# Optimization experiments

Hardware: AMD Instinct MI355X
Metric: run time of the kernel (lower is better)

Reference implementation:

```python
import jax, jax.numpy as jnp
import numpy as np

EPS = 1e-5


def setup_inputs() -> dict:
    key = jax.random.key(0)
    ks = jax.random.split(key, 6)
    BS, N, C, D, E = 4, 2048, 8, 128, 256
    x = jax.random.normal(ks[0], (BS, N, C, D), dtype=jnp.float32)
    h_prev = jax.random.normal(ks[1], (BS, C, E), dtype=jnp.float32)
    gamma = jnp.ones((C, D), dtype=jnp.float32)
    beta = jnp.zeros((C, D), dtype=jnp.float32)
    w_in = jax.random.normal(ks[2], (C, D, 2 * E), dtype=jnp.float32) * (D ** -0.5)
    b_in = jnp.zeros((C, 2 * E), dtype=jnp.float32)
    w_out = jax.random.normal(ks[3], (C, E, D), dtype=jnp.float32) * (E ** -0.5)
    b_out = jnp.zeros((C, D), dtype=jnp.float32)
    return {"x": x, "h_prev": h_prev, "gamma": gamma, "beta": beta,
            "w_in": w_in, "b_in": b_in, "w_out": w_out, "b_out": b_out}


def _scan_combine(c1, c2):
    # (a1, b1) then (a2, b2): h = a2*(a1*h + b1) + b2
    a1, b1 = c1
    a2, b2 = c2
    return a2 * a1, a2 * b1 + b2


def reference(x, h_prev, gamma, beta, w_in, b_in, w_out, b_out):
    # Grouped LayerNorm over D_col per group c
    mu = jnp.mean(x, axis=-1, keepdims=True)
    var = jnp.mean(jnp.square(x - mu), axis=-1, keepdims=True)
    x_norm = (x - mu) * jax.lax.rsqrt(var + EPS) * gamma + beta  # [BS,N,C,D]

    # Grouped linear in: [BS,N,C,D] x [C,D,2E] -> [BS,N,C,2E]
    ab = jnp.einsum('bncd,cde->bnce', x_norm, w_in) + b_in
    a_raw, b_raw = jnp.split(ab, 2, axis=-1)
    a = jax.nn.sigmoid(a_raw)           # decay gates in [0,1]
    b = jax.nn.silu(b_raw)              # gated inputs

    # Fold initial state into first step: h_1 = a_1*h0 + b_1
    b = b.at[:, 0].add(a[:, 0] * h_prev)

    # Parallel linear recurrence h_t = a_t*h_{t-1} + b_t over time axis
    _, h = jax.lax.associative_scan(_scan_combine, (a, b), axis=1)  # [BS,N,C,E]

    # Grouped linear out + residual
    out = jnp.einsum('bnce,ced->bncd', h, w_out) + b_out + x
    return out, h[:, -1]
```

## Files before the change

### kernel.cpp

```cpp
#include <hip/hip_runtime.h>
#include <hip/hip_bf16.h>

#define BS 4
#define NSEQ 2048
#define C_ 8
#define D_ 128
#define E_ 256
#define TWO_E 512
#define CHUNK 64
#define NCH (NSEQ / CHUNK)

typedef __attribute__((ext_vector_type(8))) short short8;
typedef __attribute__((ext_vector_type(4))) float floatx4;

__device__ __forceinline__ unsigned short f2bf(float f) {
    unsigned int u = __float_as_uint(f);
    return (unsigned short)((u + 0x7FFFu + ((u >> 16) & 1u)) >> 16);
}

__device__ __forceinline__ float sigmoidf_(float v) {
    return 1.0f / (1.0f + __expf(-v));
}

__global__ __launch_bounds__(256) void k_transpose_win(const float* __restrict__ w,
                                                       unsigned short* __restrict__ wt) {
    __shared__ float tile[32][33];
    const int c = blockIdx.z;
    const int d0 = blockIdx.y * 32;
    const int e0 = blockIdx.x * 32;
    const int tx = threadIdx.x, ty = threadIdx.y;
    #pragma unroll
    for (int k = 0; k < 4; k++)
        tile[ty + k * 8][tx] = w[((size_t)(c * D_ + d0 + ty + k * 8)) * TWO_E + e0 + tx];
    __syncthreads();
    #pragma unroll
    for (int k = 0; k < 4; k++)
        wt[((size_t)(c * TWO_E + e0 + ty + k * 8)) * D_ + d0 + tx] = f2bf(tile[tx][ty + k * 8]);
}

__global__ __launch_bounds__(256) void k_transpose_wout(const float* __restrict__ w,
                                                        unsigned short* __restrict__ wt) {
    __shared__ float tile[32][33];
    const int c = blockIdx.z;
    const int e0 = blockIdx.y * 32;
    const int d0 = blockIdx.x * 32;
    const int tx = threadIdx.x, ty = threadIdx.y;
    #pragma unroll
    for (int k = 0; k < 4; k++)
        tile[ty + k * 8][tx] = w[((size_t)(c * E_ + e0 + ty + k * 8)) * D_ + d0 + tx];
    __syncthreads();
    #pragma unroll
    for (int k = 0; k < 4; k++)
        wt[((size_t)(c * D_ + d0 + ty + k * 8)) * E_ + e0 + tx] = f2bf(tile[tx][ty + k * 8]);
}

__global__ __launch_bounds__(256) void k1_ln_gemm_in(
    const float* __restrict__ x, const float* __restrict__ gamma, const float* __restrict__ beta,
    const unsigned short* __restrict__ wt_in, const float* __restrict__ b_in,
    float* __restrict__ ab_buf, float* __restrict__ aggA, float* __restrict__ aggB)
{
    constexpr int LDA = 136;
    __shared__ unsigned short xn[CHUNK * LDA];

    const int gid = blockIdx.x;
    const int j = gid & (NCH - 1);
    const int c = (gid >> 5) & (C_ - 1);
    const int b = gid >> 8;
    const int n0 = j * CHUNK;
    const int tid = threadIdx.x;

    {
        const int r = tid >> 2;
        const int p = tid & 3;
        const float* xrow = x + ((size_t)((b * NSEQ + n0 + r) * C_) + c) * D_;
        float4 xv[8];
        float s = 0.f, ss = 0.f;
        #pragma unroll
        for (int i = 0; i < 8; i++) {
            xv[i] = ((const float4*)xrow)[p + 4 * i];
            s += xv[i].x + xv[i].y + xv[i].z + xv[i].w;
            ss += xv[i].x * xv[i].x + xv[i].y * xv[i].y + xv[i].z * xv[i].z + xv[i].w * xv[i].w;
        }
        s += __shfl_xor(s, 1);  s += __shfl_xor(s, 2);
        ss += __shfl_xor(ss, 1); ss += __shfl_xor(ss, 2);
        const float mu = s * (1.0f / D_);
        const float rsig = rsqrtf(fmaxf(ss * (1.0f / D_) - mu * mu, 0.f) + 1e-5f);
        #pragma unroll
        for (int i = 0; i < 8; i++) {
            const int f = p + 4 * i;
            const float4 g  = ((const float4*)(gamma + c * D_))[f];
            const float4 bt = ((const float4*)(beta + c * D_))[f];
            ushort4 o;
            o.x = f2bf((xv[i].x - mu) * rsig * g.x + bt.x);
            o.y = f2bf((xv[i].y - mu) * rsig * g.y + bt.y);
            o.z = f2bf((xv[i].z - mu) * rsig * g.z + bt.z);
            o.w = f2bf((xv[i].w - mu) * rsig * g.w + bt.w);
            *(ushort4*)&xn[r * LDA + 4 * f] = o;
        }
    }
    __syncthreads();

    const int wave = tid >> 6;
    const int lane = tid & 63;
    const int lrow = lane & 15;
    const int quad = lane >> 4;

    short8 afr[4][4];
    #pragma unroll
    for (int m = 0; m < 4; m++) {
        #pragma unroll
        for (int k = 0; k < 4; k++)
            afr[m][k] = *(const short8*)&xn[(m * 16 + lrow) * LDA + k * 32 + quad * 8];
    }

    const unsigned short* wbase = wt_in + (size_t)c * TWO_E * D_;
    float* abrow0 = ab_buf + ((size_t)(b * C_ + c) * NSEQ + n0) * TWO_E;

    #pragma unroll
    for (int nt = 0; nt < 8; nt++) {
        const int e2 = wave * 128 + nt * 16 + lrow;
        short8 bfr[4];
        #pragma unroll
        for (int k = 0; k < 4; k++)
            bfr[k] = *(const short8*)&wbase[(size_t)e2 * D_ + k * 32 + quad * 8];
        floatx4 acc[4];
        #pragma unroll
        for (int m = 0; m < 4; m++) acc[m] = (floatx4){0.f, 0.f, 0.f, 0.f};
        #pragma unroll
        for (int m = 0; m < 4; m++) {
            #pragma unroll
            for (int k = 0; k < 4; k++)
                acc[m] = __builtin_amdgcn_mfma_f32_16x16x32_bf16(afr[m][k], bfr[k], acc[m], 0, 0, 0);
        }
        const float bias = b_in[c * TWO_E + e2];
        const int col = (e2 < E_) ? (2 * e2) : (2 * (e2 - E_) + 1);
        #pragma unroll
        for (int m = 0; m < 4; m++) {
            #pragma unroll
            for (int rr = 0; rr < 4; rr++) {
                const int row = m * 16 + quad * 4 + rr;
                const float v = acc[m][rr] + bias;
                const float sg = sigmoidf_(v);
                abrow0[(size_t)row * TWO_E + col] = (e2 < E_) ? sg : (v * sg);
            }
        }
    }

    __threadfence_block();
    __syncthreads();

    {
        const int e = tid;
        float A = 1.f, Bv = 0.f;
        const float* pr = abrow0 + 2 * e;
        #pragma unroll 8
        for (int i = 0; i < CHUNK; i++) {
            const float2 v = *(const float2*)&pr[(size_t)i * TWO_E];
            A = v.x * A;
            Bv = v.x * Bv + v.y;
        }
        const size_t o = ((size_t)(b * C_ + c) * NCH + j) * E_ + e;
        aggA[o] = A;
        aggB[o] = Bv;
    }
}

__global__ __launch_bounds__(256) void k2_scan_chunks(
    const float* __restrict__ h_prev, const float* __restrict__ aggA, const float* __restrict__ aggB,
    float* __restrict__ hin, float* __restrict__ h_last)
{
    const int bc = blockIdx.x;
    const int e = threadIdx.x;
    float h = h_prev[(size_t)bc * E_ + e];
    const size_t base = (size_t)bc * NCH * E_ + e;
    #pragma unroll
    for (int jj = 0; jj < NCH; jj++) {
        hin[base + (size_t)jj * E_] = h;
        h = aggA[base + (size_t)jj * E_] * h + aggB[base + (size_t)jj * E_];
    }
    h_last[(size_t)bc * E_ + e] = h;
}

__global__ __launch_bounds__(256) void k3_scan_gemm_out(
    const float* __restrict__ ab_buf, const float* __restrict__ hin,
    const unsigned short* __restrict__ wt_out, const float* __restrict__ b_out,
    const float* __restrict__ x, float* __restrict__ out)
{
    constexpr int LDH = 264;
    __shared__ unsigned short hs[CHUNK * LDH];

    const int gid = blockIdx.x;
    const int j = gid & (NCH - 1);
    const int c = (gid >> 5) & (C_ - 1);
    const int b = gid >> 8;
    const int n0 = j * CHUNK;
    const int tid = threadIdx.x;

    {
        const int e = tid;
        float h = hin[((size_t)(b * C_ + c) * NCH + j) * E_ + e];
        const float* pr = ab_buf + ((size_t)(b * C_ + c) * NSEQ + n0) * TWO_E + 2 * e;
        #pragma unroll
        for (int i = 0; i < CHUNK; i++) {
            const float2 v = *(const float2*)&pr[(size_t)i * TWO_E];
            h = v.x * h + v.y;
            hs[i * LDH + e] = f2bf(h);
        }
    }
    __syncthreads();

    const int wave = tid >> 6;
    const int lane = tid & 63;
    const int lrow = lane & 15;
    const int quad = lane >> 4;
    const int m0 = wave * 16;

    short8 afr[8];
    #pragma unroll
    for (int k = 0; k < 8; k++)
        afr[k] = *(const short8*)&hs[(m0 + lrow) * LDH + k * 32 + quad * 8];

    const unsigned short* wbase = wt_out + (size_t)c * D_ * E_;

    #pragma unroll
    for (int nt = 0; nt < 8; nt++) {
        const int d = nt * 16 + lrow;
        short8 bfr[8];
        #pragma unroll
        for (int k = 0; k < 8; k++)
            bfr[k] = *(const short8*)&wbase[(size_t)d * E_ + k * 32 + quad * 8];
        floatx4 acc = (floatx4){0.f, 0.f, 0.f, 0.f};
        #pragma unroll
        for (int k = 0; k < 8; k++)
            acc = __builtin_amdgcn_mfma_f32_16x16x32_bf16(afr[k], bfr[k], acc, 0, 0, 0);
        const float bias = b_out[c * D_ + d];
        #pragma unroll
        for (int rr = 0; rr < 4; rr++) {
            const int row = m0 + quad * 4 + rr;
            const size_t xi = ((size_t)((b * NSEQ + n0 + row) * C_) + c) * D_ + d;
            out[xi] = acc[rr] + bias + x[xi];
        }
    }
}

extern "C" void kernel_launch(void* const* d_in, const int* in_sizes, int n_in,
                              void* d_out, int out_size, void* d_ws, size_t ws_size,
                              hipStream_t stream) {
    (void)in_sizes; (void)n_in; (void)out_size; (void)ws_size;
    const float* x      = (const float*)d_in[0];
    const float* h_prev = (const float*)d_in[1];
    const float* gamma  = (const float*)d_in[2];
    const float* beta   = (const float*)d_in[3];
    const float* w_in   = (const float*)d_in[4];
    const float* b_in   = (const float*)d_in[5];
    const float* w_out  = (const float*)d_in[6];
    const float* b_out  = (const float*)d_in[7];

    float* out    = (float*)d_out;
    float* h_last = out + (size_t)BS * NSEQ * C_ * D_;

    float* ws = (float*)d_ws;
    size_t off = 0;
    float* ab_buf = ws + off; off += (size_t)BS * C_ * NSEQ * TWO_E;
    float* aggA   = ws + off; off += (size_t)BS * C_ * NCH * E_;
    float* aggB   = ws + off; off += (size_t)BS * C_ * NCH * E_;
    float* hin    = ws + off; off += (size_t)BS * C_ * NCH * E_;
    unsigned short* wt_in  = (unsigned short*)(ws + off); off += (size_t)C_ * TWO_E * D_ / 2;
    unsigned short* wt_out = (unsigned short*)(ws + off); off += (size_t)C_ * D_ * E_ / 2;

    k_transpose_win <<<dim3(16, 4, 8), dim3(32, 8), 0, stream>>>(w_in, wt_in);
    k_transpose_wout<<<dim3(4, 8, 8),  dim3(32, 8), 0, stream>>>(w_out, wt_out);
    k1_ln_gemm_in   <<<BS * C_ * NCH, 256, 0, stream>>>(x, gamma, beta, wt_in, b_in,
                                                        ab_buf, aggA, aggB);
    k2_scan_chunks  <<<BS * C_, 256, 0, stream>>>(h_prev, aggA, aggB, hin, h_last);
    k3_scan_gemm_out<<<BS * C_ * NCH, 256, 0, stream>>>(ab_buf, hin, wt_out, b_out, x, out);
}
```

Measured before the change: 209.4 us.

## Recompute input projection in output kernel to drop ab_buf round-trip

The first kernel no longer writes the full gate/input buffer to global memory; it computes the per-chunk aggregates directly from MFMA accumulators with in-register and cross-lane shuffle composition. The final kernel recomputes LayerNorm and the input GEMM per 64-wide E slice, runs the chunk-local scan in shared memory, and accumulates the output GEMM incrementally. This removes the large fp32 intermediate write and read (~134MB) at the cost of doing the LN and input GEMM twice and serialising the scan to 64 threads per slice.

```diff
diff --git a/kernel.cpp b/kernel.cpp
--- a/kernel.cpp
+++ b/kernel.cpp
@@ -17,9 +17,41 @@
     unsigned int u = __float_as_uint(f);
     return (unsigned short)((u + 0x7FFFu + ((u >> 16) & 1u)) >> 16);
 }
-
 __device__ __forceinline__ float sigmoidf_(float v) {
     return 1.0f / (1.0f + __expf(-v));
+}
+
+__device__ __forceinline__ void layernorm_tile(
+    const float* __restrict__ x, const float* __restrict__ gamma, const float* __restrict__ beta,
+    int b, int c, int n0, int tid, unsigned short* __restrict__ xn)
+{
+    const int r = tid >> 2;
+    const int p = tid & 3;
+    const float* xrow = x + ((size_t)((b * NSEQ + n0 + r) * C_) + c) * D_;
+    float4 xv[8];
+    float s = 0.f, ss = 0.f;
+    #pragma unroll
+    for (int i = 0; i < 8; i++) {
+        xv[i] = ((const float4*)xrow)[p + 4 * i];
+        s += xv[i].x + xv[i].y + xv[i].z + xv[i].w;
+        ss += xv[i].x * xv[i].x + xv[i].y * xv[i].y + xv[i].z * xv[i].z + xv[i].w * xv[i].w;
+    }
+    s += __shfl_xor(s, 1);  s += __shfl_xor(s, 2);
+    ss += __shfl_xor(ss, 1); ss += __shfl_xor(ss, 2);
+    const float mu = s * (1.0f / D_);
+    const float rsig = rsqrtf(fmaxf(ss * (1.0f / D_) - mu * mu, 0.f) + 1e-5f);
+    #pragma unroll
+    for (int i = 0; i < 8; i++) {
+        const int f = p + 4 * i;
+        const float4 g  = ((const float4*)(gamma + c * D_))[f];
+        const float4 bt = ((const float4*)(beta + c * D_))[f];
+        ushort4 o;
+        o.x = f2bf((xv[i].x - mu) * rsig * g.x + bt.x);
+        o.y = f2bf((xv[i].y - mu) * rsig * g.y + bt.y);
+        o.z = f2bf((xv[i].z - mu) * rsig * g.z + bt.z);
+        o.w = f2bf((xv[i].w - mu) * rsig * g.w + bt.w);
+        *(ushort4*)&xn[r * 136 + 4 * f] = o;
+    }
 }
 
 __global__ __launch_bounds__(256) void k_transpose_win(const float* __restrict__ w,
@@ -54,10 +86,10 @@
         wt[((size_t)(c * D_ + d0 + ty + k * 8)) * E_ + e0 + tx] = f2bf(tile[tx][ty + k * 8]);
 }
 
-__global__ __launch_bounds__(256) void k1_ln_gemm_in(
+__global__ __launch_bounds__(256) void k1_agg(
     const float* __restrict__ x, const float* __restrict__ gamma, const float* __restrict__ beta,
     const unsigned short* __restrict__ wt_in, const float* __restrict__ b_in,
-    float* __restrict__ ab_buf, float* __restrict__ aggA, float* __restrict__ aggB)
+    float* __restrict__ aggA, float* __restrict__ aggB)
 {
     constexpr int LDA = 136;
     __shared__ unsigned short xn[CHUNK * LDA];
@@ -69,35 +101,7 @@
     const int n0 = j * CHUNK;
     const int tid = threadIdx.x;
 
-    {
-        const int r = tid >> 2;
-        const int p = tid & 3;
-        const float* xrow = x + ((size_t)((b * NSEQ + n0 + r) * C_) + c) * D_;
-        float4 xv[8];
-        float s = 0.f, ss = 0.f;
-        #pragma unroll
-        for (int i = 0; i < 8; i++) {
-            xv[i] = ((const float4*)xrow)[p + 4 * i];
-            s += xv[i].x + xv[i].y + xv[i].z + xv[i].w;
-            ss += xv[i].x * xv[i].x + xv[i].y * xv[i].y + xv[i].z * xv[i].z + xv[i].w * xv[i].w;
-        }
-        s += __shfl_xor(s, 1);  s += __shfl_xor(s, 2);
-        ss += __shfl_xor(ss, 1); ss += __shfl_xor(ss, 2);
-        const float mu = s * (1.0f / D_);
-        const float rsig = rsqrtf(fmaxf(ss * (1.0f / D_) - mu * mu, 0.f) + 1e-5f);
-        #pragma unroll
-        for (int i = 0; i < 8; i++) {
-            const int f = p + 4 * i;
-            const float4 g  = ((const float4*)(gamma + c * D_))[f];
-            const float4 bt = ((const float4*)(beta + c * D_))[f];
-            ushort4 o;
-            o.x = f2bf((xv[i].x - mu) * rsig * g.x + bt.x);
-            o.y = f2bf((xv[i].y - mu) * rsig * g.y + bt.y);
-            o.z = f2bf((xv[i].z - mu) * rsig * g.z + bt.z);
-            o.w = f2bf((xv[i].w - mu) * rsig * g.w + bt.w);
-            *(ushort4*)&xn[r * LDA + 4 * f] = o;
-        }
-    }
+    layernorm_tile(x, gamma, beta, b, c, n0, tid, xn);
     __syncthreads();
 
     const int wave = tid >> 6;
@@ -107,61 +111,63 @@
 
     short8 afr[4][4];
     #pragma unroll
-    for (int m = 0; m < 4; m++) {
+    for (int m = 0; m < 4; m++)
         #pragma unroll
         for (int k = 0; k < 4; k++)
             afr[m][k] = *(const short8*)&xn[(m * 16 + lrow) * LDA + k * 32 + quad * 8];
-    }
-
-    const unsigned short* wbase = wt_in + (size_t)c * TWO_E * D_;
-    float* abrow0 = ab_buf + ((size_t)(b * C_ + c) * NSEQ + n0) * TWO_E;
-
-    #pragma unroll
-    for (int nt = 0; nt < 8; nt++) {
-        const int e2 = wave * 128 + nt * 16 + lrow;
-        short8 bfr[4];
-        #pragma unroll
-        for (int k = 0; k < 4; k++)
-            bfr[k] = *(const short8*)&wbase[(size_t)e2 * D_ + k * 32 + quad * 8];
-        floatx4 acc[4];
-        #pragma unroll
-        for (int m = 0; m < 4; m++) acc[m] = (floatx4){0.f, 0.f, 0.f, 0.f};
+
+    const unsigned short* wbi = wt_in + (size_t)c * TWO_E * D_;
+    const size_t aggbase = ((size_t)(b * C_ + c) * NCH + j) * E_;
+
+    #pragma unroll
+    for (int p = 0; p < 4; p++) {
+        const int ea = wave * 64 + p * 16 + lrow;
+        const int eb = E_ + ea;
+        short8 bfa[4], bfb[4];
+        #pragma unroll
+        for (int k = 0; k < 4; k++) {
+            bfa[k] = *(const short8*)&wbi[(size_t)ea * D_ + k * 32 + quad * 8];
+            bfb[k] = *(const short8*)&wbi[(size_t)eb * D_ + k * 32 + quad * 8];
+        }
+        floatx4 accA[4], accB[4];
+        #pragma unroll
+        for (int m = 0; m < 4; m++) { accA[m] = (floatx4){0,0,0,0}; accB[m] = (floatx4){0,0,0,0}; }
+        #pragma unroll
+        for (int m = 0; m < 4; m++)
+            #pragma unroll
+            for (int k = 0; k < 4; k++) {
+                accA[m] = __builtin_amdgcn_mfma_f32_16x16x32_bf16(afr[m][k], bfa[k], accA[m], 0, 0, 0);
+                accB[m] = __builtin_amdgcn_mfma_f32_16x16x32_bf16(afr[m][k], bfb[k], accB[m], 0, 0, 0);
+            }
+        const float biasa = b_in[c * TWO_E + ea];
+        const float biasb = b_in[c * TWO_E + eb];
+
+        float Ac = 1.f, Bc = 0.f;
         #pragma unroll
         for (int m = 0; m < 4; m++) {
-            #pragma unroll
-            for (int k = 0; k < 4; k++)
-                acc[m] = __builtin_amdgcn_mfma_f32_16x16x32_bf16(afr[m][k], bfr[k], acc[m], 0, 0, 0);
-        }
-        const float bias = b_in[c * TWO_E + e2];
-        const int col = (e2 < E_) ? (2 * e2) : (2 * (e2 - E_) + 1);
-        #pragma unroll
-        for (int m = 0; m < 4; m++) {
+            float A = 1.f, B = 0.f;
             #pragma unroll
             for (int rr = 0; rr < 4; rr++) {
-                const int row = m * 16 + quad * 4 + rr;
-                const float v = acc[m][rr] + bias;
-                const float sg = sigmoidf_(v);
-                abrow0[(size_t)row * TWO_E + col] = (e2 < E_) ? sg : (v * sg);
-            }
-        }
-    }
-
-    __threadfence_block();
-    __syncthreads();
-
-    {
-        const int e = tid;
-        float A = 1.f, Bv = 0.f;
-        const float* pr = abrow0 + 2 * e;
-        #pragma unroll 8
-        for (int i = 0; i < CHUNK; i++) {
-            const float2 v = *(const float2*)&pr[(size_t)i * TWO_E];
-            A = v.x * A;
-            Bv = v.x * Bv + v.y;
-        }
-        const size_t o = ((size_t)(b * C_ + c) * NCH + j) * E_ + e;
-        aggA[o] = A;
-        aggB[o] = Bv;
+                const float av = sigmoidf_(accA[m][rr] + biasa);
+                const float rv = accB[m][rr] + biasb;
+                const float bv = rv * sigmoidf_(rv);
+                A = av * A;
+                B = av * B + bv;
+            }
+            #pragma unroll
+            for (int s = 16; s <= 32; s <<= 1) {
+                const float Ap = __shfl_xor(A, s);
+                const float Bp = __shfl_xor(B, s);
+                B = (lane & s) ? (A * Bp + B) : (Ap * B + Bp);
+                A = A * Ap;
+            }
+            Bc = A * Bc + B;
+            Ac = A * Ac;
+        }
+        if (quad == 0) {
+            aggA[aggbase + ea] = Ac;
+            aggB[aggbase + ea] = Bc;
+        }
     }
 }
 
@@ -181,13 +187,19 @@
     h_last[(size_t)bc * E_ + e] = h;
 }
 
-__global__ __launch_bounds__(256) void k3_scan_gemm_out(
-    const float* __restrict__ ab_buf, const float* __restrict__ hin,
+__global__ __launch_bounds__(256) void k3_fused(
+    const float* __restrict__ x, const float* __restrict__ gamma, const float* __restrict__ beta,
+    const unsigned short* __restrict__ wt_in, const float* __restrict__ b_in,
+    const float* __restrict__ hin,
     const unsigned short* __restrict__ wt_out, const float* __restrict__ b_out,
-    const float* __restrict__ x, float* __restrict__ out)
+    float* __restrict__ out)
 {
-    constexpr int LDH = 264;
-    __shared__ unsigned short hs[CHUNK * LDH];
+    constexpr int LDX = 136;
+    constexpr int LDAB = 65;
+    constexpr int LDQ = 68;
+    __shared__ unsigned short xn[CHUNK * LDX];
+    __shared__ float2 abq[CHUNK * LDAB];
+    __shared__ unsigned short hq[CHUNK * LDQ];
 
     const int gid = blockIdx.x;
     const int j = gid & (NCH - 1);
@@ -196,17 +208,7 @@
     const int n0 = j * CHUNK;
     const int tid = threadIdx.x;
 
-    {
-        const int e = tid;
-        float h = hin[((size_t)(b * C_ + c) * NCH + j) * E_ + e];
-        const float* pr = ab_buf + ((size_t)(b * C_ + c) * NSEQ + n0) * TWO_E + 2 * e;
-        #pragma unroll
-        for (int i = 0; i < CHUNK; i++) {
-            const float2 v = *(const float2*)&pr[(size_t)i * TWO_E];
-            h = v.x * h + v.y;
-            hs[i * LDH + e] = f2bf(h);
-        }
-    }
+    layernorm_tile(x, gamma, beta, b, c, n0, tid, xn);
     __syncthreads();
 
     const int wave = tid >> 6;
@@ -215,30 +217,93 @@
     const int quad = lane >> 4;
     const int m0 = wave * 16;
 
-    short8 afr[8];
-    #pragma unroll
-    for (int k = 0; k < 8; k++)
-        afr[k] = *(const short8*)&hs[(m0 + lrow) * LDH + k * 32 + quad * 8];
-
-    const unsigned short* wbase = wt_out + (size_t)c * D_ * E_;
+    const unsigned short* wbi = wt_in + (size_t)c * TWO_E * D_;
+    const unsigned short* wbo = wt_out + (size_t)c * D_ * E_;
+    const size_t hinbase = ((size_t)(b * C_ + c) * NCH + j) * E_;
+
+    floatx4 acco[8];
+    #pragma unroll
+    for (int nt = 0; nt < 8; nt++) acco[nt] = (floatx4){0, 0, 0, 0};
+
+    #pragma unroll
+    for (int q = 0; q < 4; q++) {
+        {
+            const int eq = wave * 16 + lrow;
+            const int ea = q * 64 + eq;
+            const int eb = E_ + ea;
+            short8 bfa[4], bfb[4];
+            #pragma unroll
+            for (int k = 0; k < 4; k++) {
+                bfa[k] = *(const short8*)&wbi[(size_t)ea * D_ + k * 32 + quad * 8];
+                bfb[k] = *(const short8*)&wbi[(size_t)eb * D_ + k * 32 + quad * 8];
+            }
+            floatx4 accA[4], accB[4];
+            #pragma unroll
+            for (int m = 0; m < 4; m++) { accA[m] = (floatx4){0,0,0,0}; accB[m] = (floatx4){0,0,0,0}; }
+            #pragma unroll
+            for (int m = 0; m < 4; m++) {
+                short8 afr[4];
+                #pragma unroll
+                for (int k = 0; k < 4; k++)
+                    afr[k] = *(const short8*)&xn[(m * 16 + lrow) * LDX + k * 32 + quad * 8];
+                #pragma unroll
+                for (int k = 0; k < 4; k++) {
+                    accA[m] = __builtin_amdgcn_mfma_f32_16x16x32_bf16(afr[k], bfa[k], accA[m], 0, 0, 0);
+                    accB[m] = __builtin_amdgcn_mfma_f32_16x16x32_bf16(afr[k], bfb[k], accB[m], 0, 0, 0);
+                }
+            }
+            const float biasa = b_in[c * TWO_E + ea];
+            const float biasb = b_in[c * TWO_E + eb];
+            #pragma unroll
+            for (int m = 0; m < 4; m++)
+                #pragma unroll
+                for (int rr = 0; rr < 4; rr++) {
+                    const int row = m * 16 + quad * 4 + rr;
+                    const float av = sigmoidf_(accA[m][rr] + biasa);
+                    const float rv = accB[m][rr] + biasb;
+                    const float bv = rv * sigmoidf_(rv);
+                    abq[row * LDAB + eq] = make_float2(av, bv);
+                }
+        }
+        __syncthreads();
+
+        if (tid < 64) {
+            float h = hin[hinbase + q * 64 + tid];
+            #pragma unroll
+            for (int i = 0; i < CHUNK; i++) {
+                const float2 v = abq[i * LDAB + tid];
+                h = v.x * h + v.y;
+                hq[i * LDQ + tid] = f2bf(h);
+            }
+        }
+        __syncthreads();
+
+        short8 af2[2];
+        #pragma unroll
+        for (int k = 0; k < 2; k++)
+            af2[k] = *(const short8*)&hq[(m0 + lrow) * LDQ + k * 32 + quad * 8];
+        #pragma unroll
+        for (int nt = 0; nt < 8; nt++) {
+            const int d = nt * 16 + lrow;
+            short8 bf2_[2];
+            #pragma unroll
+            for (int k = 0; k < 2; k++)
+                bf2_[k] = *(const short8*)&wbo[(size_t)d * E_ + q * 64 + k * 32 + quad * 8];
+            #pragma unroll
+            for (int k = 0; k < 2; k++)
+                acco[nt] = __builtin_amdgcn_mfma_f32_16x16x32_bf16(af2[k], bf2_[k], acco[nt], 0, 0, 0);
+        }
+    }
 
     #pragma unroll
     for (int nt = 0; nt < 8; nt++) {
         const int d = nt * 16 + lrow;
-        short8 bfr[8];
-        #pragma unroll
-        for (int k = 0; k < 8; k++)
-            bfr[k] = *(const short8*)&wbase[(size_t)d * E_ + k * 32 + quad * 8];
-        floatx4 acc = (floatx4){0.f, 0.f, 0.f, 0.f};
-        #pragma unroll
-        for (int k = 0; k < 8; k++)
-            acc = __builtin_amdgcn_mfma_f32_16x16x32_bf16(afr[k], bfr[k], acc, 0, 0, 0);
         const float bias = b_out[c * D_ + d];
         #pragma unroll
         for (int rr = 0; rr < 4; rr++) {
             const int row = m0 + quad * 4 + rr;
             const size_t xi = ((size_t)((b * NSEQ + n0 + row) * C_) + c) * D_ + d;
-            out[xi] = acc[rr] + bias + x[xi];
+            out[xi] = acco[nt][rr] + bias + x[xi];
         }
     }
 }
@@ -261,17 +326,16 @@
 
     float* ws = (float*)d_ws;
     size_t off = 0;
-    float* ab_buf = ws + off; off += (size_t)BS * C_ * NSEQ * TWO_E;
-    float* aggA   = ws + off; off += (size_t)BS * C_ * NCH * E_;
-    float* aggB   = ws + off; off += (size_t)BS * C_ * NCH * E_;
-    float* hin    = ws + off; off += (size_t)BS * C_ * NCH * E_;
+    float* aggA = ws + off; off += (size_t)BS * C_ * NCH * E_;
+    float* aggB = ws + off; off += (size_t)BS * C_ * NCH * E_;
+    float* hin  = ws + off; off += (size_t)BS * C_ * NCH * E_;
     unsigned short* wt_in  = (unsigned short*)(ws + off); off += (size_t)C_ * TWO_E * D_ / 2;
     unsigned short* wt_out = (unsigned short*)(ws + off); off += (size_t)C_ * D_ * E_ / 2;
 
     k_transpose_win <<<dim3(16, 4, 8), dim3(32, 8), 0, stream>>>(w_in, wt_in);
     k_transpose_wout<<<dim3(4, 8, 8),  dim3(32, 8), 0, stream>>>(w_out, wt_out);
-    k1_ln_gemm_in   <<<BS * C_ * NCH, 256, 0, stream>>>(x, gamma, beta, wt_in, b_in,
-                                                        ab_buf, aggA, aggB);
+    k1_agg          <<<BS * C_ * NCH, 256, 0, stream>>>(x, gamma, beta, wt_in, b_in, aggA, aggB);
     k2_scan_chunks  <<<BS * C_, 256, 0, stream>>>(h_prev, aggA, aggB, hin, h_last);
-    k3_scan_gemm_out<<<BS * C_ * NCH, 256, 0, stream>>>(ab_buf, hin, wt_out, b_out, x, out);
-}
+    k3_fused        <<<BS * C_ * NCH, 256, 0, stream>>>(x, gamma, beta, wt_in, b_in,
+                                                        hin, wt_out, b_out, out);
+}
```

After: 201.9 us. -3.6%, faster.
